# Optimization experiments

Measured on AMD Instinct MI355X. Metric: run time of the kernel, lower is better.

The kernel has to match this reference:

```python
import jax, jax.numpy as jnp
import numpy as np

N = 50000
E = 800000
IN = 128
HID = 64
HEADS = 4
OUT = 128
NEG_SLOPE = 0.2


def _segment_softmax(logits, seg, num_segments):
    # logits: (E, H), seg: (E,) destination node ids
    m = jax.ops.segment_max(logits, seg, num_segments=num_segments)
    m = jnp.where(jnp.isfinite(m), m, 0.0)
    e = jnp.exp(logits - m[seg])
    s = jax.ops.segment_sum(e, seg, num_segments=num_segments)
    return e / (s[seg] + 1e-16)


def _gat_conv(x, edge_index, W, att_src, att_dst, bias, heads, out_ch, concat):
    # PyG GATConv with add_self_loops=True, negative_slope=0.2 (eval mode: no dropout)
    n = x.shape[0]
    loops = jnp.arange(n, dtype=edge_index.dtype)
    src = jnp.concatenate([edge_index[0], loops])
    dst = jnp.concatenate([edge_index[1], loops])
    h = (x @ W).reshape(n, heads, out_ch)                      # (N, H, C)
    a_src = jnp.einsum('nhc,hc->nh', h, att_src)               # (N, H)
    a_dst = jnp.einsum('nhc,hc->nh', h, att_dst)
    logits = jax.nn.leaky_relu(a_src[src] + a_dst[dst], NEG_SLOPE)  # (E', H)
    alpha = _segment_softmax(logits, dst, n)                   # (E', H)
    msg = alpha[:, :, None] * h[src]                           # (E', H, C)
    out = jax.ops.segment_sum(msg, dst, num_segments=n)        # (N, H, C)
    if concat:
        out = out.reshape(n, heads * out_ch)
    else:
        out = out.mean(axis=1)
    return out + bias


def setup_inputs() -> dict:
    key = jax.random.key(0)
    ks = jax.random.split(key, 16)
    hc = HID * HEADS
    s = 0.1
    return {
        'x': jax.random.normal(ks[0], (N, IN), dtype=jnp.float32),
        'edge_index': jax.random.randint(ks[1], (2, E), 0, N, dtype=jnp.int64),
        'W1': jax.random.normal(ks[2], (IN, hc), dtype=jnp.float32) * s,
        'att_src1': jax.random.normal(ks[3], (HEADS, HID), dtype=jnp.float32) * s,
        'att_dst1': jax.random.normal(ks[4], (HEADS, HID), dtype=jnp.float32) * s,
        'b1': jnp.zeros((hc,), dtype=jnp.float32),
        'lin1_w': jax.random.normal(ks[5], (IN, hc), dtype=jnp.float32) * s,
        'lin1_b': jnp.zeros((hc,), dtype=jnp.float32),
        'W2': jax.random.normal(ks[6], (hc, OUT), dtype=jnp.float32) * s,
        'att_src2': jax.random.normal(ks[7], (1, OUT), dtype=jnp.float32) * s,
        'att_dst2': jax.random.normal(ks[8], (1, OUT), dtype=jnp.float32) * s,
        'b2': jnp.zeros((OUT,), dtype=jnp.float32),
        'lin2_w': jax.random.normal(ks[9], (hc, OUT), dtype=jnp.float32) * s,
        'lin2_b': jnp.zeros((OUT,), dtype=jnp.float32),
    }


def reference(x, edge_index, W1, att_src1, att_dst1, b1, lin1_w, lin1_b,
              W2, att_src2, att_dst2, b2, lin2_w, lin2_b):
    # h1 = ELU(GATConv1(x) + Linear1(x))  (dropout is eval-mode no-op)
    h = _gat_conv(x, edge_index, W1, att_src1, att_dst1, b1, HEADS, HID, True)
    h = jax.nn.elu(h + x @ lin1_w + lin1_b)
    # out = GATConv2(h) + Linear2(h)
    o = _gat_conv(h, edge_index, W2, att_src2, att_dst2, b2, 1, OUT, False)
    return o + h @ lin2_w + lin2_b
```

## Files before the change

### kernel.cpp

```cpp
#include <hip/hip_runtime.h>
#include <math.h>

#define N_NODES 50000
#define N_EDGES 800000
#define EP (N_EDGES + N_NODES)
#define IN_CH 128
#define HID 64
#define HEADS 4
#define HC (HID * HEADS)
#define OUT_CH 128
#define NEG_SLOPE 0.2f
#define NSCAN ((N_NODES + 255) / 256)
#define MTILES (N_NODES / 16)

typedef __bf16 bf16x8 __attribute__((ext_vector_type(8)));
typedef float  f32x4  __attribute__((ext_vector_type(4)));

__device__ __forceinline__ float bf2f(unsigned short u) {
    return __uint_as_float(((unsigned)u) << 16);
}
__device__ __forceinline__ unsigned short f2bf(float f) {
    unsigned u = __float_as_uint(f);
    return (unsigned short)((u + 0x7fffu + ((u >> 16) & 1u)) >> 16);
}
__device__ __forceinline__ float lrelu(float v) {
    return v > 0.f ? v : NEG_SLOPE * v;
}
__device__ __forceinline__ bf16x8 ldfrag(const unsigned short* p) {
    uint4 u = *(const uint4*)p;
    return __builtin_bit_cast(bf16x8, u);
}

__global__ void hist_kernel(const int* __restrict__ ei, int* __restrict__ cnt) {
    int e = blockIdx.x * 256 + threadIdx.x;
    if (e >= EP) return;
    int d = (e < N_EDGES) ? ei[N_EDGES + e] : e - N_EDGES;
    atomicAdd(&cnt[d], 1);
}

__global__ void scan1_kernel(const int* __restrict__ cnt,
                             int* __restrict__ row, int* __restrict__ bsum) {
    __shared__ int buf[256];
    int i = blockIdx.x * 256 + threadIdx.x;
    int v = (i < N_NODES) ? cnt[i] : 0;
    buf[threadIdx.x] = v;
    __syncthreads();
#pragma unroll
    for (int off = 1; off < 256; off <<= 1) {
        int t = (threadIdx.x >= off) ? buf[threadIdx.x - off] : 0;
        __syncthreads();
        buf[threadIdx.x] += t;
        __syncthreads();
    }
    if (i < N_NODES) row[i] = buf[threadIdx.x] - v;
    if (threadIdx.x == 255) bsum[blockIdx.x] = buf[255];
}

__global__ void scan2_kernel(const int* __restrict__ bsum,
                             int* __restrict__ boff, int* __restrict__ rowN) {
    __shared__ int buf[256];
    int tid = threadIdx.x;
    int v = (tid < NSCAN) ? bsum[tid] : 0;
    buf[tid] = v;
    __syncthreads();
#pragma unroll
    for (int off = 1; off < 256; off <<= 1) {
        int t = (tid >= off) ? buf[tid - off] : 0;
        __syncthreads();
        buf[tid] += t;
        __syncthreads();
    }
    if (tid < NSCAN) boff[tid] = buf[tid] - v;
    if (tid == 255) rowN[0] = buf[255];
}

__global__ void scan3_kernel(int* __restrict__ row, const int* __restrict__ boff,
                             int* __restrict__ pos) {
    int i = blockIdx.x * 256 + threadIdx.x;
    if (i >= N_NODES) return;
    int r = row[i] + boff[blockIdx.x];
    row[i] = r;
    pos[i] = r;
}

__global__ void scatter_el1_kernel(const int* __restrict__ ei,
                                   int* __restrict__ pos,
                                   const float4* __restrict__ AS4,
                                   const float4* __restrict__ AD4,
                                   int* __restrict__ adjS, int* __restrict__ adjD,
                                   float4* __restrict__ EL4) {
    int e = blockIdx.x * 256 + threadIdx.x;
    if (e >= EP) return;
    int s, d;
    if (e < N_EDGES) { s = ei[e]; d = ei[N_EDGES + e]; }
    else             { s = d = e - N_EDGES; }
    int p = atomicAdd(&pos[d], 1);
    adjS[p] = s;
    adjD[p] = d;
    float4 a = AS4[s], b = AD4[d];
    float4 o;
    o.x = expf(lrelu(a.x + b.x));
    o.y = expf(lrelu(a.y + b.y));
    o.z = expf(lrelu(a.z + b.z));
    o.w = expf(lrelu(a.w + b.w));
    EL4[p] = o;
}

__global__ void convx_kernel(const float* __restrict__ x,
                             unsigned short* __restrict__ xb) {
    int i = blockIdx.x * 256 + threadIdx.x;
    if (i >= N_NODES * (IN_CH / 4)) return;
    float4 v = ((const float4*)x)[i];
    ushort4 o;
    o.x = f2bf(v.x); o.y = f2bf(v.y); o.z = f2bf(v.z); o.w = f2bf(v.w);
    ((ushort4*)xb)[i] = o;
}

__global__ void pack12_kernel(const float* __restrict__ W1,
                              const float* __restrict__ L1,
                              const float* __restrict__ W2,
                              const float* __restrict__ L2,
                              unsigned short* __restrict__ Bp1,
                              unsigned short* __restrict__ Bp2) {
    int t = blockIdx.x * 256 + threadIdx.x;
    if (t < 8192) {
        int frag = t >> 6, l = t & 63;
        int ks = frag >> 5, nf = frag & 31;
        int col = nf * 16 + (l & 15);
        int kb = ks * 32 + (l >> 4) * 8;
        unsigned short* o = Bp1 + (size_t)t * 8;
#pragma unroll
        for (int i = 0; i < 8; ++i) {
            int k = kb + i;
            float v = (col < HC) ? W1[k * HC + col] : L1[k * HC + (col - HC)];
            o[i] = f2bf(v);
        }
    } else if (t < 16384) {
        int u = t - 8192;
        int frag = u >> 6, l = u & 63;
        int ks = frag >> 4, nf = frag & 15;
        int col = nf * 16 + (l & 15);
        int kb = ks * 32 + (l >> 4) * 8;
        unsigned short* o = Bp2 + (size_t)u * 8;
#pragma unroll
        for (int i = 0; i < 8; ++i) {
            int k = kb + i;
            float v = (col < OUT_CH) ? W2[k * OUT_CH + col]
                                     : L2[k * OUT_CH + (col - OUT_CH)];
            o[i] = f2bf(v);
        }
    }
}

__global__ __launch_bounds__(256) void gemm1_mfma(
        const unsigned short* __restrict__ xb,
        const unsigned short* __restrict__ Bp,
        const float* __restrict__ as1, const float* __restrict__ ad1,
        unsigned short* __restrict__ H1b, unsigned short* __restrict__ XLb,
        float* __restrict__ AS, float* __restrict__ AD) {
    __shared__ float sAS[16][4], sAD[16][4];
    int m0 = blockIdx.x * 16;
    int w = threadIdx.x >> 6, l = threadIdx.x & 63;
    int arow = m0 + (l & 15);
    int koff = (l >> 4) * 8;
    f32x4 acc[8];
#pragma unroll
    for (int f = 0; f < 8; ++f) acc[f] = (f32x4){0.f, 0.f, 0.f, 0.f};
#pragma unroll
    for (int ks = 0; ks < 4; ++ks) {
        bf16x8 a = ldfrag(xb + (size_t)arow * IN_CH + ks * 32 + koff);
        const unsigned short* bb = Bp + ((size_t)((ks * 32 + w * 8) * 64 + l)) * 8;
#pragma unroll
        for (int f = 0; f < 8; ++f) {
            bf16x8 b = ldfrag(bb + (size_t)f * 512);
            acc[f] = __builtin_amdgcn_mfma_f32_16x16x32_bf16(a, b, acc[f], 0, 0, 0);
        }
    }
    int g = l >> 4, lc = l & 15;
#pragma unroll
    for (int f = 0; f < 8; ++f) {
        int col = w * 128 + f * 16 + lc;
#pragma unroll
        for (int r = 0; r < 4; ++r) {
            int m = m0 + g * 4 + r;
            float v = acc[f][r];
            if (col < HC) H1b[(size_t)m * HC + col] = f2bf(v);
            else          XLb[(size_t)m * HC + (col - HC)] = f2bf(v);
        }
    }
    if (w < 2) {
        float ps[4][2], pd[4][2];
#pragma unroll
        for (int r = 0; r < 4; ++r) { ps[r][0]=ps[r][1]=pd[r][0]=pd[r][1]=0.f; }
#pragma unroll
        for (int f = 0; f < 8; ++f) {
            int col = w * 128 + f * 16 + lc;
            float av = as1[col], dv = ad1[col];
            int hp = f >> 2;
#pragma unroll
            for (int r = 0; r < 4; ++r) {
                ps[r][hp] += acc[f][r] * av;
                pd[r][hp] += acc[f][r] * dv;
            }
        }
#pragma unroll
        for (int msk = 1; msk < 16; msk <<= 1)
#pragma unroll
            for (int r = 0; r < 4; ++r) {
                ps[r][0] += __shfl_xor(ps[r][0], msk, 64);
                ps[r][1] += __shfl_xor(ps[r][1], msk, 64);
                pd[r][0] += __shfl_xor(pd[r][0], msk, 64);
                pd[r][1] += __shfl_xor(pd[r][1], msk, 64);
            }
        if (lc == 0)
#pragma unroll
            for (int r = 0; r < 4; ++r) {
                sAS[g * 4 + r][w * 2 + 0] = ps[r][0];
                sAS[g * 4 + r][w * 2 + 1] = ps[r][1];
                sAD[g * 4 + r][w * 2 + 0] = pd[r][0];
                sAD[g * 4 + r][w * 2 + 1] = pd[r][1];
            }
    }
    __syncthreads();
    int t = threadIdx.x;
    if (t < 64)       AS[(m0 + (t >> 2)) * 4 + (t & 3)] = sAS[t >> 2][t & 3];
    else if (t < 128) { int u = t - 64;
                        AD[(m0 + (u >> 2)) * 4 + (u & 3)] = sAD[u >> 2][u & 3]; }
}

__global__ __launch_bounds__(256) void gemm2_mfma(
        const unsigned short* __restrict__ HBb,
        const unsigned short* __restrict__ Bp,
        const float* __restrict__ as2, const float* __restrict__ ad2,
        unsigned short* __restrict__ H2b, unsigned short* __restrict__ XLb,
        float* __restrict__ AS, float* __restrict__ AD) {
    __shared__ float sAS[16][2], sAD[16][2];
    int m0 = blockIdx.x * 16;
    int w = threadIdx.x >> 6, l = threadIdx.x & 63;
    int arow = m0 + (l & 15);
    int koff = (l >> 4) * 8;
    f32x4 acc[4];
#pragma unroll
    for (int f = 0; f < 4; ++f) acc[f] = (f32x4){0.f, 0.f, 0.f, 0.f};
#pragma unroll
    for (int ks = 0; ks < 8; ++ks) {
        bf16x8 a = ldfrag(HBb + (size_t)arow * HC + ks * 32 + koff);
        const unsigned short* bb = Bp + ((size_t)((ks * 16 + w * 4) * 64 + l)) * 8;
#pragma unroll
        for (int f = 0; f < 4; ++f) {
            bf16x8 b = ldfrag(bb + (size_t)f * 512);
            acc[f] = __builtin_amdgcn_mfma_f32_16x16x32_bf16(a, b, acc[f], 0, 0, 0);
        }
    }
    int g = l >> 4, lc = l & 15;
#pragma unroll
    for (int f = 0; f < 4; ++f) {
        int col = w * 64 + f * 16 + lc;
#pragma unroll
        for (int r = 0; r < 4; ++r) {
            int m = m0 + g * 4 + r;
            float v = acc[f][r];
            if (col < OUT_CH) H2b[(size_t)m * OUT_CH + col] = f2bf(v);
            else              XLb[(size_t)m * OUT_CH + (col - OUT_CH)] = f2bf(v);
        }
    }
    if (w < 2) {
        float ps[4], pd[4];
#pragma unroll
        for (int r = 0; r < 4; ++r) { ps[r] = 0.f; pd[r] = 0.f; }
#pragma unroll
        for (int f = 0; f < 4; ++f) {
            int col = w * 64 + f * 16 + lc;
            float av = as2[col], dv = ad2[col];
#pragma unroll
            for (int r = 0; r < 4; ++r) {
                ps[r] += acc[f][r] * av;
                pd[r] += acc[f][r] * dv;
            }
        }
#pragma unroll
        for (int msk = 1; msk < 16; msk <<= 1)
#pragma unroll
            for (int r = 0; r < 4; ++r) {
                ps[r] += __shfl_xor(ps[r], msk, 64);
                pd[r] += __shfl_xor(pd[r], msk, 64);
            }
        if (lc == 0)
#pragma unroll
            for (int r = 0; r < 4; ++r) {
                sAS[g * 4 + r][w] = ps[r];
                sAD[g * 4 + r][w] = pd[r];
            }
    }
    __syncthreads();
    int t = threadIdx.x;
    if (t < 16)       AS[m0 + t] = sAS[t][0] + sAS[t][1];
    else if (t < 32)  { int u = t - 16; AD[m0 + u] = sAD[u][0] + sAD[u][1]; }
}

__global__ void el2_kernel(const int* __restrict__ adjS,
                           const int* __restrict__ adjD,
                           const float* __restrict__ AS,
                           const float* __restrict__ AD,
                           float* __restrict__ EL) {
    int p = blockIdx.x * 256 + threadIdx.x;
    if (p >= EP) return;
    EL[p] = expf(lrelu(AS[adjS[p]] + AD[adjD[p]]));
}

__global__ void gather1_kernel(const int* __restrict__ row,
                               const int* __restrict__ adjS,
                               const float4* __restrict__ EL4,
                               const unsigned short* __restrict__ H1b,
                               const unsigned short* __restrict__ XLb,
                               const float* __restrict__ b1,
                               const float* __restrict__ l1b,
                               unsigned short* __restrict__ HBb) {
    int d = blockIdx.x, j = threadIdx.x;
    int hh = j >> 4;
    int beg = row[d], end = row[d + 1];
    const ushort4* Hr = (const ushort4*)H1b;
    float a0 = 0.f, a1 = 0.f, a2 = 0.f, a3 = 0.f, esum = 0.f;
    int i = beg;
    for (; i + 8 <= end; i += 8) {
        int sa[8]; float ea[8]; ushort4 qa[8];
#pragma unroll
        for (int k = 0; k < 8; ++k) sa[k] = adjS[i + k];
#pragma unroll
        for (int k = 0; k < 8; ++k) {
            float4 t = EL4[i + k];
            ea[k] = hh < 2 ? (hh == 0 ? t.x : t.y) : (hh == 2 ? t.z : t.w);
        }
#pragma unroll
        for (int k = 0; k < 8; ++k) qa[k] = Hr[(size_t)sa[k] * 64 + j];
#pragma unroll
        for (int k = 0; k < 8; ++k) {
            a0 += ea[k] * bf2f(qa[k].x); a1 += ea[k] * bf2f(qa[k].y);
            a2 += ea[k] * bf2f(qa[k].z); a3 += ea[k] * bf2f(qa[k].w);
            esum += ea[k];
        }
    }
    for (; i < end; ++i) {
        int s = adjS[i];
        float4 t = EL4[i];
        float e = hh < 2 ? (hh == 0 ? t.x : t.y) : (hh == 2 ? t.z : t.w);
        ushort4 q = Hr[(size_t)s * 64 + j];
        a0 += e * bf2f(q.x); a1 += e * bf2f(q.y);
        a2 += e * bf2f(q.z); a3 += e * bf2f(q.w);
        esum += e;
    }
    float inv = 1.f / (esum + 1e-16f);
    ushort4 xq = ((const ushort4*)XLb)[(size_t)d * 64 + j];
    float4 bb = ((const float4*)b1)[j];
    float4 lb = ((const float4*)l1b)[j];
    float v0 = a0 * inv + bf2f(xq.x) + bb.x + lb.x;
    float v1 = a1 * inv + bf2f(xq.y) + bb.y + lb.y;
    float v2 = a2 * inv + bf2f(xq.z) + bb.z + lb.z;
    float v3 = a3 * inv + bf2f(xq.w) + bb.w + lb.w;
    v0 = v0 > 0.f ? v0 : expm1f(v0);
    v1 = v1 > 0.f ? v1 : expm1f(v1);
    v2 = v2 > 0.f ? v2 : expm1f(v2);
    v3 = v3 > 0.f ? v3 : expm1f(v3);
    ushort4 o;
    o.x = f2bf(v0); o.y = f2bf(v1); o.z = f2bf(v2); o.w = f2bf(v3);
    ((ushort4*)HBb)[(size_t)d * 64 + j] = o;
}

__global__ void gather2_kernel(const int* __restrict__ row,
                               const int* __restrict__ adjS,
                               const float* __restrict__ EL,
                               const unsigned short* __restrict__ H2b,
                               const unsigned short* __restrict__ XLb,
                               const float* __restrict__ b2,
                               const float* __restrict__ l2b,
                               float* __restrict__ out) {
    int d = blockIdx.x, l = threadIdx.x;
    int beg = row[d], end = row[d + 1];
    const ushort2* Hr = (const ushort2*)H2b;
    float ax = 0.f, ay = 0.f, esum = 0.f;
    int i = beg;
    for (; i + 8 <= end; i += 8) {
        int sa[8]; float ea[8]; ushort2 qa[8];
#pragma unroll
        for (int k = 0; k < 8; ++k) sa[k] = adjS[i + k];
#pragma unroll
        for (int k = 0; k < 8; ++k) ea[k] = EL[i + k];
#pragma unroll
        for (int k = 0; k < 8; ++k) qa[k] = Hr[(size_t)sa[k] * 64 + l];
#pragma unroll
        for (int k = 0; k < 8; ++k) {
            ax += ea[k] * bf2f(qa[k].x);
            ay += ea[k] * bf2f(qa[k].y);
            esum += ea[k];
        }
    }
    for (; i < end; ++i) {
        int s = adjS[i];
        float e = EL[i];
        ushort2 q = Hr[(size_t)s * 64 + l];
        ax += e * bf2f(q.x); ay += e * bf2f(q.y);
        esum += e;
    }
    float inv = 1.f / (esum + 1e-16f);
    ushort2 xq = ((const ushort2*)XLb)[(size_t)d * 64 + l];
    float2 bb = ((const float2*)b2)[l];
    float2 lb = ((const float2*)l2b)[l];
    ((float2*)out)[(size_t)d * 64 + l] =
        make_float2(ax * inv + bf2f(xq.x) + bb.x + lb.x,
                    ay * inv + bf2f(xq.y) + bb.y + lb.y);
}

extern "C" void kernel_launch(void* const* d_in, const int* in_sizes, int n_in,
                              void* d_out, int out_size, void* d_ws, size_t ws_size,
                              hipStream_t stream) {
    const float* x    = (const float*)d_in[0];
    const int*   ei   = (const int*)d_in[1];
    const float* W1   = (const float*)d_in[2];
    const float* as1  = (const float*)d_in[3];
    const float* ad1  = (const float*)d_in[4];
    const float* b1   = (const float*)d_in[5];
    const float* l1w  = (const float*)d_in[6];
    const float* l1b  = (const float*)d_in[7];
    const float* W2   = (const float*)d_in[8];
    const float* as2  = (const float*)d_in[9];
    const float* ad2  = (const float*)d_in[10];
    const float* b2   = (const float*)d_in[11];
    const float* l2w  = (const float*)d_in[12];
    const float* l2b  = (const float*)d_in[13];
    float* out = (float*)d_out;

    float* ws = (float*)d_ws;
    unsigned short* xb  = (unsigned short*)ws;
    float* fp = ws + (size_t)N_NODES * 64;
    unsigned short* H1b = (unsigned short*)fp;
    fp += (size_t)N_NODES * 128;
    unsigned short* XLb = (unsigned short*)fp;
    fp += (size_t)N_NODES * 128;
    unsigned short* HBb = (unsigned short*)fp;
    fp += (size_t)N_NODES * 128;
    float* AS1 = fp; fp += (size_t)N_NODES * HEADS;
    float* AD1 = fp; fp += (size_t)N_NODES * HEADS;
    float* AS2 = fp; fp += N_NODES;
    float* AD2 = fp; fp += N_NODES;
    float* EL1 = fp; fp += (size_t)EP * 4;
    unsigned short* Bp1 = (unsigned short*)fp; fp += 32768;
    unsigned short* Bp2 = (unsigned short*)fp; fp += 32768;
    int* cnt  = (int*)fp;
    int* row  = cnt + N_NODES;
    int* pos  = row + N_NODES + 1;
    int* bsum = pos + N_NODES;
    int* boff = bsum + NSCAN;
    int* adjS = boff + NSCAN;
    int* adjD = adjS + EP;
    unsigned short* H2b = H1b;
    unsigned short* XL2b = XLb;
    float* EL2 = EL1;

    int nE = (EP + 255) / 256;

    hipMemsetAsync(cnt, 0, N_NODES * 4, stream);
    hist_kernel<<<nE, 256, 0, stream>>>(ei, cnt);
    scan1_kernel<<<NSCAN, 256, 0, stream>>>(cnt, row, bsum);
    scan2_kernel<<<1, 256, 0, stream>>>(bsum, boff, row + N_NODES);
    scan3_kernel<<<NSCAN, 256, 0, stream>>>(row, boff, pos);

    convx_kernel<<<(N_NODES * (IN_CH / 4) + 255) / 256, 256, 0, stream>>>(x, xb);
    pack12_kernel<<<64, 256, 0, stream>>>(W1, l1w, W2, l2w, Bp1, Bp2);

    gemm1_mfma<<<MTILES, 256, 0, stream>>>(xb, Bp1, as1, ad1, H1b, XLb, AS1, AD1);
    scatter_el1_kernel<<<nE, 256, 0, stream>>>(ei, pos, (const float4*)AS1,
                                               (const float4*)AD1, adjS, adjD,
                                               (float4*)EL1);
    gather1_kernel<<<N_NODES, 64, 0, stream>>>(row, adjS, (const float4*)EL1,
                                               H1b, XLb, b1, l1b, HBb);

    gemm2_mfma<<<MTILES, 256, 0, stream>>>(HBb, Bp2, as2, ad2, H2b, XL2b, AS2, AD2);
    el2_kernel<<<nE, 256, 0, stream>>>(adjS, adjD, AS2, AD2, EL2);
    gather2_kernel<<<N_NODES, 64, 0, stream>>>(row, adjS, EL2, H2b, XL2b,
                                               b2, l2b, out);
}
```

Baseline: 280.0 us.

## Fuse x bf16 conversion into gemm1 and deepen gather unrolling

Removes the separate convx kernel: gemm1 now loads fp32 x directly and converts it to bf16 in registers before the MFMA, which saves one launch and a full write and re-read of the bf16 copy. The gather kernels gain a 16-edge unrolled loop ahead of the 8-edge loop, giving more independent loads in flight. They also hoist the XL/bias loads to the start of the kernel so those loads overlap the edge loop. The trade-off is higher register pressure in the gathers and, in gemm1, twice the A-operand bytes read from global memory.

```diff
diff --git a/kernel.cpp b/kernel.cpp
--- a/kernel.cpp
+++ b/kernel.cpp
@@ -15,6 +15,7 @@
 
 typedef __bf16 bf16x8 __attribute__((ext_vector_type(8)));
 typedef float  f32x4  __attribute__((ext_vector_type(4)));
+typedef unsigned short u16x8 __attribute__((ext_vector_type(8)));
 
 __device__ __forceinline__ float bf2f(unsigned short u) {
     return __uint_as_float(((unsigned)u) << 16);
@@ -29,6 +30,12 @@
 __device__ __forceinline__ bf16x8 ldfrag(const unsigned short* p) {
     uint4 u = *(const uint4*)p;
     return __builtin_bit_cast(bf16x8, u);
+}
+__device__ __forceinline__ bf16x8 packA(float4 v0, float4 v1) {
+    u16x8 t;
+    t[0] = f2bf(v0.x); t[1] = f2bf(v0.y); t[2] = f2bf(v0.z); t[3] = f2bf(v0.w);
+    t[4] = f2bf(v1.x); t[5] = f2bf(v1.y); t[6] = f2bf(v1.z); t[7] = f2bf(v1.w);
+    return __builtin_bit_cast(bf16x8, t);
 }
 
 __global__ void hist_kernel(const int* __restrict__ ei, int* __restrict__ cnt) {
@@ -106,16 +113,6 @@
     EL4[p] = o;
 }
 
-__global__ void convx_kernel(const float* __restrict__ x,
-                             unsigned short* __restrict__ xb) {
-    int i = blockIdx.x * 256 + threadIdx.x;
-    if (i >= N_NODES * (IN_CH / 4)) return;
-    float4 v = ((const float4*)x)[i];
-    ushort4 o;
-    o.x = f2bf(v.x); o.y = f2bf(v.y); o.z = f2bf(v.z); o.w = f2bf(v.w);
-    ((ushort4*)xb)[i] = o;
-}
-
 __global__ void pack12_kernel(const float* __restrict__ W1,
                               const float* __restrict__ L1,
                               const float* __restrict__ W2,
@@ -153,7 +150,7 @@
 }
 
 __global__ __launch_bounds__(256) void gemm1_mfma(
-        const unsigned short* __restrict__ xb,
+        const float* __restrict__ x,
         const unsigned short* __restrict__ Bp,
         const float* __restrict__ as1, const float* __restrict__ ad1,
         unsigned short* __restrict__ H1b, unsigned short* __restrict__ XLb,
@@ -163,12 +160,15 @@
     int w = threadIdx.x >> 6, l = threadIdx.x & 63;
     int arow = m0 + (l & 15);
     int koff = (l >> 4) * 8;
+    const float* xrow = x + (size_t)arow * IN_CH + koff;
     f32x4 acc[8];
 #pragma unroll
     for (int f = 0; f < 8; ++f) acc[f] = (f32x4){0.f, 0.f, 0.f, 0.f};
 #pragma unroll
     for (int ks = 0; ks < 4; ++ks) {
-        bf16x8 a = ldfrag(xb + (size_t)arow * IN_CH + ks * 32 + koff);
+        float4 v0 = *(const float4*)(xrow + ks * 32);
+        float4 v1 = *(const float4*)(xrow + ks * 32 + 4);
+        bf16x8 a = packA(v0, v1);
         const unsigned short* bb = Bp + ((size_t)((ks * 32 + w * 8) * 64 + l)) * 8;
 #pragma unroll
         for (int f = 0; f < 8; ++f) {
@@ -319,9 +319,30 @@
     int d = blockIdx.x, j = threadIdx.x;
     int hh = j >> 4;
     int beg = row[d], end = row[d + 1];
+    ushort4 xq = ((const ushort4*)XLb)[(size_t)d * 64 + j];
+    float4 bb = ((const float4*)b1)[j];
+    float4 lb = ((const float4*)l1b)[j];
     const ushort4* Hr = (const ushort4*)H1b;
     float a0 = 0.f, a1 = 0.f, a2 = 0.f, a3 = 0.f, esum = 0.f;
     int i = beg;
+    for (; i + 16 <= end; i += 16) {
+        int sa[16]; float ea[16]; ushort4 qa[16];
+#pragma unroll
+        for (int k = 0; k < 16; ++k) sa[k] = adjS[i + k];
+#pragma unroll
+        for (int k = 0; k < 16; ++k) {
+            float4 t = EL4[i + k];
+            ea[k] = hh < 2 ? (hh == 0 ? t.x : t.y) : (hh == 2 ? t.z : t.w);
+        }
+#pragma unroll
+        for (int k = 0; k < 16; ++k) qa[k] = Hr[(size_t)sa[k] * 64 + j];
+#pragma unroll
+        for (int k = 0; k < 16; ++k) {
+            a0 += ea[k] * bf2f(qa[k].x); a1 += ea[k] * bf2f(qa[k].y);
+            a2 += ea[k] * bf2f(qa[k].z); a3 += ea[k] * bf2f(qa[k].w);
+            esum += ea[k];
+        }
+    }
     for (; i + 8 <= end; i += 8) {
         int sa[8]; float ea[8]; ushort4 qa[8];
 #pragma unroll
@@ -350,9 +371,6 @@
         esum += e;
     }
     float inv = 1.f / (esum + 1e-16f);
-    ushort4 xq = ((const ushort4*)XLb)[(size_t)d * 64 + j];
-    float4 bb = ((const float4*)b1)[j];
-    float4 lb = ((const float4*)l1b)[j];
     float v0 = a0 * inv + bf2f(xq.x) + bb.x + lb.x;
     float v1 = a1 * inv + bf2f(xq.y) + bb.y + lb.y;
     float v2 = a2 * inv + bf2f(xq.z) + bb.z + lb.z;
@@ -376,9 +394,27 @@
                                float* __restrict__ out) {
     int d = blockIdx.x, l = threadIdx.x;
     int beg = row[d], end = row[d + 1];
+    ushort2 xq = ((const ushort2*)XLb)[(size_t)d * 64 + l];
+    float2 bb = ((const float2*)b2)[l];
+    float2 lb = ((const float2*)l2b)[l];
     const ushort2* Hr = (const ushort2*)H2b;
     float ax = 0.f, ay = 0.f, esum = 0.f;
     int i = beg;
+    for (; i + 16 <= end; i += 16) {
+        int sa[16]; float ea[16]; ushort2 qa[16];
+#pragma unroll
+        for (int k = 0; k < 16; ++k) sa[k] = adjS[i + k];
+#pragma unroll
+        for (int k = 0; k < 16; ++k) ea[k] = EL[i + k];
+#pragma unroll
+        for (int k = 0; k < 16; ++k) qa[k] = Hr[(size_t)sa[k] * 64 + l];
+#pragma unroll
+        for (int k = 0; k < 16; ++k) {
+            ax += ea[k] * bf2f(qa[k].x);
+            ay += ea[k] * bf2f(qa[k].y);
+            esum += ea[k];
+        }
+    }
     for (; i + 8 <= end; i += 8) {
         int sa[8]; float ea[8]; ushort2 qa[8];
 #pragma unroll
@@ -402,9 +438,6 @@
         esum += e;
     }
     float inv = 1.f / (esum + 1e-16f);
-    ushort2 xq = ((const ushort2*)XLb)[(size_t)d * 64 + l];
-    float2 bb = ((const float2*)b2)[l];
-    float2 lb = ((const float2*)l2b)[l];
     ((float2*)out)[(size_t)d * 64 + l] =
         make_float2(ax * inv + bf2f(xq.x) + bb.x + lb.x,
                     ay * inv + bf2f(xq.y) + bb.y + lb.y);
@@ -430,8 +463,7 @@
     float* out = (float*)d_out;
 
     float* ws = (float*)d_ws;
-    unsigned short* xb  = (unsigned short*)ws;
-    float* fp = ws + (size_t)N_NODES * 64;
+    float* fp = ws;
     unsigned short* H1b = (unsigned short*)fp;
     fp += (size_t)N_NODES * 128;
     unsigned short* XLb = (unsigned short*)fp;
@@ -464,10 +496,9 @@
     scan2_kernel<<<1, 256, 0, stream>>>(bsum, boff, row + N_NODES);
     scan3_kernel<<<NSCAN, 256, 0, stream>>>(row, boff, pos);
 
-    convx_kernel<<<(N_NODES * (IN_CH / 4) + 255) / 256, 256, 0, stream>>>(x, xb);
     pack12_kernel<<<64, 256, 0, stream>>>(W1, l1w, W2, l2w, Bp1, Bp2);
 
-    gemm1_mfma<<<MTILES, 256, 0, stream>>>(xb, Bp1, as1, ad1, H1b, XLb, AS1, AD1);
+    gemm1_mfma<<<MTILES, 256, 0, stream>>>(x, Bp1, as1, ad1, H1b, XLb, AS1, AD1);
     scatter_el1_kernel<<<nE, 256, 0, stream>>>(ei, pos, (const float4*)AS1,
                                                (const float4*)AD1, adjS, adjD,
                                                (float4*)EL1);
```

Measured after the change: 280.8 us. Within noise of the previous version (+0.3%).
